# Kernel tuning notes

Measured on AMD Instinct MI355X. Metric: run time of the kernel, lower is better.

## Reference

```python
import jax, jax.numpy as jnp
import numpy as np

V, BLK, L, H, C, FF = 50257, 2048, 6, 8, 512, 2048
D = C // H  # head_dim = 64

def setup_inputs() -> dict:
    key = jax.random.key(0)
    ks = jax.random.split(key, 16)
    s = 0.02
    proj_std = 0.02 / np.sqrt(2 * L)
    return {
        'idx': jax.random.randint(ks[0], (2, 2048), 0, V, dtype=jnp.int64),
        'wte': jax.random.normal(ks[1], (V, C), jnp.float32) * s,
        'wpe': jax.random.normal(ks[2], (BLK, C), jnp.float32) * s,
        'ln1_w': jnp.ones((L, C), jnp.float32), 'ln1_b': jnp.zeros((L, C), jnp.float32),
        'c_attn_w': jax.random.normal(ks[3], (L, 3 * C, C), jnp.float32) * s,
        'c_proj_w': jax.random.normal(ks[4], (L, C, C), jnp.float32) * proj_std,
        'ln2_w': jnp.ones((L, C), jnp.float32), 'ln2_b': jnp.zeros((L, C), jnp.float32),
        'fc_w': jax.random.normal(ks[5], (L, FF, C), jnp.float32) * s,
        'proj_w': jax.random.normal(ks[6], (L, C, FF), jnp.float32) * proj_std,
        'lnf_w': jnp.ones((C,), jnp.float32), 'lnf_b': jnp.zeros((C,), jnp.float32),
    }

def _layernorm(x, w, b, eps=1e-5):
    mu = jnp.mean(x, axis=-1, keepdims=True)
    var = jnp.var(x, axis=-1, keepdims=True)
    return (x - mu) * jax.lax.rsqrt(var + eps) * w + b

def _attn(x, attn_w, proj_w, mask):
    B, T, _ = x.shape
    qkv = jnp.einsum('btc,fc->btf', x, attn_w)  # (B,T,3C)
    q, k, v = jnp.split(qkv, 3, axis=-1)
    q = q.reshape(B, T, H, D)
    k = k.reshape(B, T, H, D)
    v = v.reshape(B, T, H, D)
    scale = 1.0 / np.sqrt(D)
    att = jnp.einsum('bthd,bshd->bhts', q, k) * scale  # (B,H,T,T)
    att = jnp.where(mask, att, -jnp.inf)
    att = jax.nn.softmax(att, axis=-1)
    y = jnp.einsum('bhts,bshd->bthd', att, v).reshape(B, T, C)
    return jnp.einsum('btc,oc->bto', y, proj_w)

def reference(idx, wte, wpe, ln1_w, ln1_b, c_attn_w, c_proj_w, ln2_w, ln2_b, fc_w, proj_w, lnf_w, lnf_b):
    B, T = idx.shape
    pos = jnp.arange(T)
    x = wte[idx] + wpe[pos]  # (B,T,C); dropout p=0
    mask = jnp.tril(jnp.ones((T, T), bool))[None, None]
    for i in range(L):
        x = x + _attn(_layernorm(x, ln1_w[i], ln1_b[i]), c_attn_w[i], c_proj_w[i], mask)
        h = _layernorm(x, ln2_w[i], ln2_b[i])
        h = jax.nn.gelu(jnp.einsum('btc,fc->btf', h, fc_w[i]), approximate=False)
        x = x + jnp.einsum('btf,cf->btc', h, proj_w[i])
    x = _layernorm(x, lnf_w, lnf_b)
    logits = jnp.einsum('btc,vc->btv', x, wte)  # tied lm_head
    return logits
```

## Files before the change

kernel.cpp:

```cpp
#include <hip/hip_runtime.h>

typedef unsigned short u16;
typedef short bf16x8 __attribute__((ext_vector_type(8)));
typedef float f32x4 __attribute__((ext_vector_type(4)));
typedef unsigned short u16x4 __attribute__((ext_vector_type(4)));
typedef unsigned short u16x8 __attribute__((ext_vector_type(8)));
typedef unsigned int u32x2 __attribute__((ext_vector_type(2)));

#define B_ 2
#define T_ 2048
#define C_ 512
#define H_ 8
#define FF_ 2048
#define L_ 6
#define V_ 50257
#define M_ (B_*T_)

__device__ __forceinline__ u16 f2b(float f) {
  union { float f; unsigned u; } v; v.f = f;
  unsigned r = v.u + 0x7FFFu + ((v.u >> 16) & 1u);
  return (u16)(r >> 16);
}
__device__ __forceinline__ float b2f(u16 u) {
  union { unsigned u; float f; } v; v.u = ((unsigned)u) << 16; return v.f;
}
__device__ __forceinline__ unsigned pk_bf16(float lo, float hi) {
  unsigned r;
  asm volatile("v_cvt_pk_bf16_f32 %0, %1, %2" : "=v"(r) : "v"(lo), "v"(hi));
  return r;
}

__device__ __forceinline__ void async16(const void* g, void* l) {
  __builtin_amdgcn_global_load_lds((const __attribute__((address_space(1))) unsigned int*)g,
                                   (__attribute__((address_space(3))) unsigned int*)l, 16, 0, 0);
}

__device__ __forceinline__ bf16x8 scale8(u16x8 v, float s) {
  union { bf16x8 b; unsigned u[4]; } r;
#pragma unroll
  for (int i = 0; i < 4; i++)
    r.u[i] = pk_bf16(b2f(v[2*i]) * s, b2f(v[2*i+1]) * s);
  return r.b;
}

struct CvtArgs { const f32x4* s[5]; u16x4* d[5]; };
__global__ void cvt_all_k(CvtArgs a) {
  const int sizes[5] = { V_*C_/4, L_*3*C_*C_/4, L_*C_*C_/4, L_*FF_*C_/4, L_*C_*FF_/4 };
  int gid = blockIdx.x * blockDim.x + threadIdx.x;
  int stride = gridDim.x * blockDim.x;
#pragma unroll
  for (int seg = 0; seg < 5; seg++) {
    const f32x4* src = a.s[seg];
    u16x4* dst = a.d[seg];
    for (int i = gid; i < sizes[seg]; i += stride) {
      f32x4 v = src[i];
      u16x4 o;
      o[0] = f2b(v[0]); o[1] = f2b(v[1]); o[2] = f2b(v[2]); o[3] = f2b(v[3]);
      dst[i] = o;
    }
  }
}

__global__ void embed_k(const int* __restrict__ idx, const float* __restrict__ wte,
                        const float* __restrict__ wpe, float* __restrict__ x) {
  int t = blockIdx.x * 256 + threadIdx.x;
  int row = t >> 7;
  int c4 = t & 127;
  int tok = idx[row];
  int pos = row & (T_ - 1);
  f32x4 a = ((const f32x4*)(wte + (long)tok * C_))[c4];
  f32x4 p = ((const f32x4*)(wpe + (long)pos * C_))[c4];
  ((f32x4*)x)[t] = a + p;
}

__global__ void ln_k(const float* __restrict__ x, const float* __restrict__ w,
                     const float* __restrict__ b, u16* __restrict__ out) {
  int wv = threadIdx.x >> 6;
  int lane = threadIdx.x & 63;
  int row = blockIdx.x * 4 + wv;
  const f32x4* xr = (const f32x4*)(x + (long)row * C_);
  f32x4 v0 = xr[lane * 2], v1 = xr[lane * 2 + 1];
  float s = 0.f, s2 = 0.f;
#pragma unroll
  for (int j = 0; j < 4; j++) { s += v0[j] + v1[j]; s2 += v0[j]*v0[j] + v1[j]*v1[j]; }
#pragma unroll
  for (int off = 32; off >= 1; off >>= 1) { s += __shfl_xor(s, off); s2 += __shfl_xor(s2, off); }
  float mu = s * (1.f / C_);
  float inv = rsqrtf(s2 * (1.f / C_) - mu * mu + 1e-5f);
  const f32x4* wr = (const f32x4*)w;
  const f32x4* br = (const f32x4*)b;
  f32x4 w0 = wr[lane*2], w1 = wr[lane*2+1], b0 = br[lane*2], b1 = br[lane*2+1];
  u16x8 o;
#pragma unroll
  for (int j = 0; j < 4; j++) {
    o[j]     = f2b((v0[j] - mu) * inv * w0[j] + b0[j]);
    o[j + 4] = f2b((v1[j] - mu) * inv * w1[j] + b1[j]);
  }
  *(u16x8*)(out + (long)row * C_ + lane * 8) = o;
}

template<int EPI, int BM>
__global__ __launch_bounds__(256) void gemm_bt_k(
    const u16* __restrict__ A, const u16* __restrict__ Bw,
    u16* __restrict__ Cb, float* __restrict__ Cf,
    int N, int K, int ldc)
{
  constexpr int MT = BM / 32;
  __shared__ __align__(16) u16 sA[2][BM * 32];
  __shared__ __align__(16) u16 sB[2][128 * 32];
  const int tid = threadIdx.x;
  const int n0 = blockIdx.x * 128;
  const int m0 = blockIdx.y * BM;
  const int w = tid >> 6;
  const int lane = tid & 63;
  const int wm = (w >> 1) * (BM / 2);
  const int wn = (w & 1) * 64;
  const int g = lane >> 4;
  const int l15 = lane & 15;

  f32x4 acc[MT][4] = {};

  const int nk = K >> 5;
  int arow0 = tid >> 2, ak0 = (tid & 3) * 8;
  int c1 = tid + 256;
  int arow1 = c1 >> 2, ak1 = (c1 & 3) * 8;
  const u16* gA0 = A + (long)(m0 + arow0) * K + ak0;
  const u16* gA1 = A + (long)(m0 + arow1) * K + ak1;
  const u16* gB0 = Bw + (long)(n0 + arow0) * K + ak0;
  const u16* gB1 = Bw + (long)(n0 + arow1) * K + ak1;
  const int lb0 = (w * 64) * 8;
  const int lb1 = (256 + w * 64) * 8;

  auto stage = [&](int buf, int kt) {
    int ko = kt << 5;
    async16(gA0 + ko, &sA[buf][lb0]);
    if constexpr (BM == 128) async16(gA1 + ko, &sA[buf][lb1]);
    async16(gB0 + ko, &sB[buf][lb0]);
    async16(gB1 + ko, &sB[buf][lb1]);
  };

  stage(0, 0);
  stage(1, 1);
  for (int kt = 0; kt < nk; kt++) {
    const int cur = kt & 1;
    if (kt + 1 < nk) {
      if constexpr (BM == 128) asm volatile("s_waitcnt vmcnt(4)" ::: "memory");
      else                     asm volatile("s_waitcnt vmcnt(3)" ::: "memory");
    } else {
      asm volatile("s_waitcnt vmcnt(0)" ::: "memory");
    }
    __builtin_amdgcn_s_barrier();
    const u16* pa = sA[cur];
    const u16* pb = sB[cur];
    bf16x8 af[MT], bfr[4];
#pragma unroll
    for (int mt = 0; mt < MT; mt++)
      af[mt] = *(const bf16x8*)(pa + (wm + mt * 16 + l15) * 32 + g * 8);
#pragma unroll
    for (int nt = 0; nt < 4; nt++)
      bfr[nt] = *(const bf16x8*)(pb + (wn + nt * 16 + l15) * 32 + g * 8);
#pragma unroll
    for (int mt = 0; mt < MT; mt++)
#pragma unroll
      for (int nt = 0; nt < 4; nt++)
        acc[mt][nt] = __builtin_amdgcn_mfma_f32_16x16x32_bf16(af[mt], bfr[nt], acc[mt][nt], 0, 0, 0);
    __builtin_amdgcn_s_barrier();
    if (kt + 2 < nk) stage(cur, kt + 2);
  }

#pragma unroll
  for (int mt = 0; mt < MT; mt++) {
    int m = m0 + wm + mt * 16 + g * 4;
#pragma unroll
    for (int nt = 0; nt < 4; nt++) {
      int n = n0 + wn + nt * 16 + l15;
      f32x4 v = acc[mt][nt];
#pragma unroll
      for (int r = 0; r < 4; r++) {
        long ci = (long)(m + r) * ldc + n;
        if (EPI == 0) {
          Cb[ci] = f2b(v[r]);
        } else if (EPI == 1) {
          Cf[ci] += v[r];
        } else {
          float f = v[r];
          f = 0.5f * f * (1.0f + erff(f * 0.70710678118654752f));
          Cb[ci] = f2b(f);
        }
      }
    }
  }
}

__global__ __launch_bounds__(512, 2) void gemm_lmhead_k(
    const u16* __restrict__ A, const u16* __restrict__ Bw,
    float* __restrict__ Cf, int N)
{
  __shared__ __align__(16) u16 sA[2][512 * 32];
  __shared__ __align__(16) u16 sB[2][128 * 32];
  const int K = 512;
  const int bid = blockIdx.x;
  const int swz = (bid & 7) * 393 + (bid >> 3);
  const int n0 = (swz % 393) * 128;
  const int m0 = (swz / 393) * 512;
  const int tid = threadIdx.x;
  const int w = tid >> 6;
  const int lane = tid & 63;
  const int wm = (w >> 1) * 128;
  const int wn = (w & 1) * 64;
  const int g = lane >> 4;
  const int l15 = lane & 15;

  f32x4 acc[8][4] = {};

  const u16* gA[4];
#pragma unroll
  for (int i = 0; i < 4; i++) {
    int c = tid + i * 512;
    gA[i] = A + (long)(m0 + (c >> 2)) * K + (c & 3) * 8;
  }
  int brow = n0 + (tid >> 2); if (brow > N - 1) brow = N - 1;
  const u16* gB0 = Bw + (long)brow * K + (tid & 3) * 8;

  auto stage = [&](int buf, int kt) {
    int ko = kt << 5;
#pragma unroll
    for (int i = 0; i < 4; i++)
      async16(gA[i] + ko, &sA[buf][(i * 512 + w * 64) * 8]);
    async16(gB0 + ko, &sB[buf][(w * 64) * 8]);
  };

  stage(0, 0);
  stage(1, 1);
  const int nk = K >> 5;
  for (int kt = 0; kt < nk; kt++) {
    const int cur = kt & 1;
    if (kt + 1 < nk) asm volatile("s_waitcnt vmcnt(5)" ::: "memory");
    else             asm volatile("s_waitcnt vmcnt(0)" ::: "memory");
    __builtin_amdgcn_s_barrier();
    const u16* pa = sA[cur];
    const u16* pb = sB[cur];
    bf16x8 af[8], bfr[4];
#pragma unroll
    for (int mt = 0; mt < 8; mt++)
      af[mt] = *(const bf16x8*)(pa + (wm + mt * 16 + l15) * 32 + g * 8);
#pragma unroll
    for (int nt = 0; nt < 4; nt++)
      bfr[nt] = *(const bf16x8*)(pb + (wn + nt * 16 + l15) * 32 + g * 8);
    __builtin_amdgcn_s_setprio(1);
#pragma unroll
    for (int mt = 0; mt < 8; mt++)
#pragma unroll
      for (int nt = 0; nt < 4; nt++)
        acc[mt][nt] = __builtin_amdgcn_mfma_f32_16x16x32_bf16(af[mt], bfr[nt], acc[mt][nt], 0, 0, 0);
    __builtin_amdgcn_s_setprio(0);
    __builtin_amdgcn_s_barrier();
    if (kt + 2 < nk) stage(cur, kt + 2);
  }

#pragma unroll
  for (int mt = 0; mt < 8; mt++) {
    int m = m0 + wm + mt * 16 + g * 4;
#pragma unroll
    for (int nt = 0; nt < 4; nt++) {
      int n = n0 + wn + nt * 16 + l15;
      f32x4 v = acc[mt][nt];
      if (n < N) {
#pragma unroll
        for (int r = 0; r < 4; r++)
          Cf[(long)(m + r) * N + n] = v[r];
      }
    }
  }
}

__global__ __launch_bounds__(128) void attn_k(const u16* __restrict__ qkv, u16* __restrict__ out) {
  const int bh = blockIdx.y;
  const int b = bh >> 3;
  const int h = bh & 7;
  const int tid = threadIdx.x;
  const int wv = tid >> 6;
  const int lane = tid & 63;
  const int g = lane >> 4;
  const int l15 = lane & 15;
  const int qblk = 31 - (blockIdx.x >> 1);
  const int halfsel = blockIdx.x & 1;

  __shared__ __align__(16) u16 Ks[2][64 * 64];
  __shared__ __align__(16) u16 Vt[2][64 * 72];
  __shared__ __align__(16) u16 Ps[2][16 * 64];

  const long base = (long)b * T_ * 1536;
  const u16* kbase = qkv + base + 512 + h * 64;
  const u16* vbase = qkv + base + 1024 + h * 64;
  const int kq = tid & 15;
  const int dg = tid >> 4;
  const float qscale = 0.18033688011112042f;

  const int q0 = qblk * 64 + halfsel * 32 + wv * 16;

  const u16* qrow = qkv + base + (long)(q0 + l15) * 1536 + h * 64;
  bf16x8 qf0 = scale8(*(const u16x8*)(qrow + g * 8), qscale);
  bf16x8 qf1 = scale8(*(const u16x8*)(qrow + 32 + g * 8), qscale);

  f32x4 o[4] = {};
  float mrun[4] = {-1e30f, -1e30f, -1e30f, -1e30f};
  float lrun[4] = {0.f, 0.f, 0.f, 0.f};
  const int kvend = qblk * 64 + 64;

  u16x8 vreg[4];
#pragma unroll
  for (int i = 0; i < 4; i++) {
    int chunk = i * 128 + tid;
    int row = chunk >> 3, c8 = chunk & 7;
    async16(kbase + (long)row * 1536 + (c8 ^ (row & 7)) * 8,
            &Ks[0][(i * 128 + wv * 64) * 8]);
  }
#pragma unroll
  for (int t = 0; t < 4; t++)
    vreg[t] = *(const u16x8*)(vbase + (long)(kq + 16 * t) * 1536 + dg * 8);
#pragma unroll
  for (int e = 0; e < 8; e++) {
    int d = dg * 8 + e;
    u32x2 wq = { (unsigned)vreg[0][e] | ((unsigned)vreg[1][e] << 16),
                 (unsigned)vreg[2][e] | ((unsigned)vreg[3][e] << 16) };
    *(u32x2*)(&Vt[0][d * 72 + kq * 4]) = wq;
  }
  __syncthreads();

  int cur = 0;
  for (int j0 = 0; j0 < kvend; j0 += 64, cur ^= 1) {
    const bool more = (j0 + 64) < kvend;
    if (more) {
      int jn = j0 + 64;
#pragma unroll
      for (int i = 0; i < 4; i++) {
        int chunk = i * 128 + tid;
        int row = chunk >> 3, c8 = chunk & 7;
        async16(kbase + (long)(jn + row) * 1536 + (c8 ^ (row & 7)) * 8,
                &Ks[cur ^ 1][(i * 128 + wv * 64) * 8]);
      }
#pragma unroll
      for (int t = 0; t < 4; t++)
        vreg[t] = *(const u16x8*)(vbase + (long)(jn + kq + 16 * t) * 1536 + dg * 8);
    }

    f32x4 s[4] = {};
    const u16* kp = Ks[cur];
#pragma unroll
    for (int t = 0; t < 4; t++) {
      int row = t * 16 + l15;
      const u16* kr = kp + row * 64;
      bf16x8 k0 = *(const bf16x8*)(kr + ((g ^ (row & 7)) * 8));
      bf16x8 k1 = *(const bf16x8*)(kr + (((4 + g) ^ (row & 7)) * 8));
      s[t] = __builtin_amdgcn_mfma_f32_16x16x32_bf16(qf0, k0, s[t], 0, 0, 0);
      s[t] = __builtin_amdgcn_mfma_f32_16x16x32_bf16(qf1, k1, s[t], 0, 0, 0);
    }

    const bool diag = (j0 + 64) == kvend;
    u16* pw = Ps[wv];
#pragma unroll
    for (int r = 0; r < 4; r++) {
      int row = q0 + g * 4 + r;
      float v0 = s[0][r], v1 = s[1][r], v2 = s[2][r], v3 = s[3][r];
      if (diag) {
        if (j0 +      l15 > row) v0 = -1e30f;
        if (j0 + 16 + l15 > row) v1 = -1e30f;
        if (j0 + 32 + l15 > row) v2 = -1e30f;
        if (j0 + 48 + l15 > row) v3 = -1e30f;
      }
      float mloc = fmaxf(fmaxf(v0, v1), fmaxf(v2, v3));
      float m = mrun[r];
      if (!__all(mloc <= m + 8.0f)) {
        float mx = mloc;
        mx = fmaxf(mx, __shfl_xor(mx, 1));
        mx = fmaxf(mx, __shfl_xor(mx, 2));
        mx = fmaxf(mx, __shfl_xor(mx, 4));
        mx = fmaxf(mx, __shfl_xor(mx, 8));
        float mn = fmaxf(m, mx);
        float sc2 = exp2f(m - mn);
        lrun[r] *= sc2;
#pragma unroll
        for (int dt = 0; dt < 4; dt++) o[dt][r] *= sc2;
        m = mn; mrun[r] = mn;
      }
      float e0 = exp2f(v0 - m), e1 = exp2f(v1 - m);
      float e2 = exp2f(v2 - m), e3 = exp2f(v3 - m);
      lrun[r] += (e0 + e1) + (e2 + e3);
      u32x2 pkq = { pk_bf16(e0, e1), pk_bf16(e2, e3) };
      int prow = g * 4 + r;
      int byt = prow * 128 + ((((l15 >> 1) ^ (prow & 7)) << 4)) + (l15 & 1) * 8;
      *(u32x2*)((char*)pw + byt) = pkq;
    }

    const u16* vt = Vt[cur];
    bf16x8 pf0 = *(const bf16x8*)((char*)pw + l15 * 128 + (((g) ^ (l15 & 7)) << 4));
    bf16x8 pf1 = *(const bf16x8*)((char*)pw + l15 * 128 + (((4 + g) ^ (l15 & 7)) << 4));
#pragma unroll
    for (int dt = 0; dt < 4; dt++) {
      int d = dt * 16 + l15;
      bf16x8 vf0 = *(const bf16x8*)(vt + d * 72 + g * 8);
      bf16x8 vf1 = *(const bf16x8*)(vt + d * 72 + 32 + g * 8);
      o[dt] = __builtin_amdgcn_mfma_f32_16x16x32_bf16(pf0, vf0, o[dt], 0, 0, 0);
      o[dt] = __builtin_amdgcn_mfma_f32_16x16x32_bf16(pf1, vf1, o[dt], 0, 0, 0);
    }

    if (more) {
#pragma unroll
      for (int e = 0; e < 8; e++) {
        int d = dg * 8 + e;
        u32x2 wq = { (unsigned)vreg[0][e] | ((unsigned)vreg[1][e] << 16),
                     (unsigned)vreg[2][e] | ((unsigned)vreg[3][e] << 16) };
        *(u32x2*)(&Vt[cur ^ 1][d * 72 + kq * 4]) = wq;
      }
    }
    __syncthreads();
  }

#pragma unroll
  for (int r = 0; r < 4; r++) {
    float ls = lrun[r];
    ls += __shfl_xor(ls, 1); ls += __shfl_xor(ls, 2);
    ls += __shfl_xor(ls, 4); ls += __shfl_xor(ls, 8);
    float inv = 1.0f / ls;
    int row = q0 + g * 4 + r;
    u16* orow = out + (long)(b * T_ + row) * C_ + h * 64;
#pragma unroll
    for (int dt = 0; dt < 4; dt++)
      orow[dt * 16 + l15] = f2b(o[dt][r] * inv);
  }
}

extern "C" void kernel_launch(void* const* d_in, const int* in_sizes, int n_in,
                              void* d_out, int out_size, void* d_ws, size_t ws_size,
                              hipStream_t stream) {
  const int*   idx    = (const int*)  d_in[0];
  const float* wte    = (const float*)d_in[1];
  const float* wpe    = (const float*)d_in[2];
  const float* ln1w   = (const float*)d_in[3];
  const float* ln1b   = (const float*)d_in[4];
  const float* wattn  = (const float*)d_in[5];
  const float* wcproj = (const float*)d_in[6];
  const float* ln2w   = (const float*)d_in[7];
  const float* ln2b   = (const float*)d_in[8];
  const float* wfc    = (const float*)d_in[9];
  const float* wproj2 = (const float*)d_in[10];
  const float* lnfw   = (const float*)d_in[11];
  const float* lnfb   = (const float*)d_in[12];
  float* out = (float*)d_out;

  char* p = (char*)d_ws;
  size_t off = 0;
  auto alloc = [&](size_t bytes) -> void* {
    void* r = p + off; off += (bytes + 255) & ~(size_t)255; return r;
  };
  float* x    = (float*)alloc((size_t)M_ * C_ * 4);
  u16* xn     = (u16*)alloc((size_t)M_ * C_ * 2);
  u16* qkvb   = (u16*)alloc((size_t)M_ * 3 * C_ * 2);
  u16* attb   = (u16*)alloc((size_t)M_ * C_ * 2);
  u16* hb     = (u16*)alloc((size_t)M_ * FF_ * 2);
  u16* wteB   = (u16*)alloc((size_t)V_ * C_ * 2);
  u16* wattnB = (u16*)alloc((size_t)L_ * 3 * C_ * C_ * 2);
  u16* wprojB = (u16*)alloc((size_t)L_ * C_ * C_ * 2);
  u16* wfcB   = (u16*)alloc((size_t)L_ * FF_ * C_ * 2);
  u16* wp2B   = (u16*)alloc((size_t)L_ * C_ * FF_ * 2);
  if (off > ws_size) return;

  CvtArgs ca;
  ca.s[0] = (const f32x4*)wte;    ca.d[0] = (u16x4*)wteB;
  ca.s[1] = (const f32x4*)wattn;  ca.d[1] = (u16x4*)wattnB;
  ca.s[2] = (const f32x4*)wcproj; ca.d[2] = (u16x4*)wprojB;
  ca.s[3] = (const f32x4*)wfc;    ca.d[3] = (u16x4*)wfcB;
  ca.s[4] = (const f32x4*)wproj2; ca.d[4] = (u16x4*)wp2B;
  cvt_all_k<<<dim3(2048), dim3(256), 0, stream>>>(ca);

  embed_k<<<dim3(M_ * C_ / 4 / 256), dim3(256), 0, stream>>>(idx, wte, wpe, x);

  for (int l = 0; l < L_; l++) {
    ln_k<<<dim3(M_ / 4), dim3(256), 0, stream>>>(x, ln1w + l * C_, ln1b + l * C_, xn);
    gemm_bt_k<0, 64><<<dim3(12, 64), dim3(256), 0, stream>>>(
        xn, wattnB + (size_t)l * 3 * C_ * C_, qkvb, nullptr, 3 * C_, C_, 3 * C_);
    attn_k<<<dim3(64, B_ * H_), dim3(128), 0, stream>>>(qkvb, attb);
    gemm_bt_k<1, 64><<<dim3(4, 64), dim3(256), 0, stream>>>(
        attb, wprojB + (size_t)l * C_ * C_, nullptr, x, C_, C_, C_);
    ln_k<<<dim3(M_ / 4), dim3(256), 0, stream>>>(x, ln2w + l * C_, ln2b + l * C_, xn);
    gemm_bt_k<2, 128><<<dim3(16, 32), dim3(256), 0, stream>>>(
        xn, wfcB + (size_t)l * FF_ * C_, hb, nullptr, FF_, C_, FF_);
    gemm_bt_k<1, 64><<<dim3(4, 64), dim3(256), 0, stream>>>(
        hb, wp2B + (size_t)l * C_ * FF_, nullptr, x, C_, FF_, C_);
  }
  ln_k<<<dim3(M_ / 4), dim3(256), 0, stream>>>(x, lnfw, lnfb, xn);
  gemm_lmhead_k<<<dim3(8 * 393), dim3(512), 0, stream>>>(xn, wteB, out, V_);
}
```

Measured before the change: 1.447 ms.

## Triple-buffer GEMM LDS pipelines and shrink tiles for proj and LM-head

Moves both GEMM kernels from double to triple LDS buffering. The next stage is now issued right after the barrier, so the trailing barrier per k-step goes away. Adds a BN template parameter so the residual projection GEMMs use 64x64 tiles, doubling their grid. The LM-head tile is halved to 256x128, which doubles its block count and drops setprio and the occupancy hint. This aims to cut barrier stalls and raise wave occupancy, at the cost of more LDS per block and less reuse per tile in the LM-head.

```diff
diff --git a/kernel.cpp b/kernel.cpp
--- a/kernel.cpp
+++ b/kernel.cpp
@@ -33,6 +33,13 @@
 __device__ __forceinline__ void async16(const void* g, void* l) {
   __builtin_amdgcn_global_load_lds((const __attribute__((address_space(1))) unsigned int*)g,
                                    (__attribute__((address_space(3))) unsigned int*)l, 16, 0, 0);
+}
+
+template<int N> __device__ __forceinline__ void vwait() {
+  if constexpr (N == 0) asm volatile("s_waitcnt vmcnt(0)" ::: "memory");
+  else if constexpr (N == 2) asm volatile("s_waitcnt vmcnt(2)" ::: "memory");
+  else if constexpr (N == 3) asm volatile("s_waitcnt vmcnt(3)" ::: "memory");
+  else if constexpr (N == 4) asm volatile("s_waitcnt vmcnt(4)" ::: "memory");
 }
 
 __device__ __forceinline__ bf16x8 scale8(u16x8 v, float s) {
@@ -99,80 +106,82 @@
   *(u16x8*)(out + (long)row * C_ + lane * 8) = o;
 }
 
-template<int EPI, int BM>
+template<int EPI, int BM, int BN>
 __global__ __launch_bounds__(256) void gemm_bt_k(
     const u16* __restrict__ A, const u16* __restrict__ Bw,
     u16* __restrict__ Cb, float* __restrict__ Cf,
     int N, int K, int ldc)
 {
   constexpr int MT = BM / 32;
-  __shared__ __align__(16) u16 sA[2][BM * 32];
-  __shared__ __align__(16) u16 sB[2][128 * 32];
+  constexpr int NT = BN / 32;
+  constexpr int AJ = BM / 64;
+  constexpr int BJ = BN / 64;
+  constexpr int LPT = AJ + BJ;
+  __shared__ __align__(16) u16 sA[3][BM * 32];
+  __shared__ __align__(16) u16 sB[3][BN * 32];
   const int tid = threadIdx.x;
-  const int n0 = blockIdx.x * 128;
+  const int n0 = blockIdx.x * BN;
   const int m0 = blockIdx.y * BM;
   const int w = tid >> 6;
   const int lane = tid & 63;
   const int wm = (w >> 1) * (BM / 2);
-  const int wn = (w & 1) * 64;
+  const int wn = (w & 1) * (BN / 2);
   const int g = lane >> 4;
   const int l15 = lane & 15;
 
-  f32x4 acc[MT][4] = {};
+  f32x4 acc[MT][NT] = {};
 
   const int nk = K >> 5;
-  int arow0 = tid >> 2, ak0 = (tid & 3) * 8;
-  int c1 = tid + 256;
-  int arow1 = c1 >> 2, ak1 = (c1 & 3) * 8;
-  const u16* gA0 = A + (long)(m0 + arow0) * K + ak0;
-  const u16* gA1 = A + (long)(m0 + arow1) * K + ak1;
-  const u16* gB0 = Bw + (long)(n0 + arow0) * K + ak0;
-  const u16* gB1 = Bw + (long)(n0 + arow1) * K + ak1;
-  const int lb0 = (w * 64) * 8;
-  const int lb1 = (256 + w * 64) * 8;
+  const int k8 = (tid & 3) * 8;
+  const u16* gA[AJ];
+  const u16* gB[BJ];
+#pragma unroll
+  for (int j = 0; j < AJ; j++)
+    gA[j] = A + (long)(m0 + (tid >> 2) + j * 64) * K + k8;
+#pragma unroll
+  for (int j = 0; j < BJ; j++)
+    gB[j] = Bw + (long)(n0 + (tid >> 2) + j * 64) * K + k8;
 
   auto stage = [&](int buf, int kt) {
     int ko = kt << 5;
-    async16(gA0 + ko, &sA[buf][lb0]);
-    if constexpr (BM == 128) async16(gA1 + ko, &sA[buf][lb1]);
-    async16(gB0 + ko, &sB[buf][lb0]);
-    async16(gB1 + ko, &sB[buf][lb1]);
+#pragma unroll
+    for (int j = 0; j < AJ; j++)
+      async16(gA[j] + ko, &sA[buf][(j * 256 + w * 64) * 8]);
+#pragma unroll
+    for (int j = 0; j < BJ; j++)
+      async16(gB[j] + ko, &sB[buf][(j * 256 + w * 64) * 8]);
   };
 
   stage(0, 0);
   stage(1, 1);
+  int cur = 0, nxt = 2;
   for (int kt = 0; kt < nk; kt++) {
-    const int cur = kt & 1;
-    if (kt + 1 < nk) {
-      if constexpr (BM == 128) asm volatile("s_waitcnt vmcnt(4)" ::: "memory");
-      else                     asm volatile("s_waitcnt vmcnt(3)" ::: "memory");
-    } else {
-      asm volatile("s_waitcnt vmcnt(0)" ::: "memory");
-    }
+    if (kt + 1 < nk) vwait<LPT>(); else vwait<0>();
     __builtin_amdgcn_s_barrier();
+    if (kt + 2 < nk) stage(nxt, kt + 2);
     const u16* pa = sA[cur];
     const u16* pb = sB[cur];
-    bf16x8 af[MT], bfr[4];
+    bf16x8 af[MT], bfr[NT];
 #pragma unroll
     for (int mt = 0; mt < MT; mt++)
       af[mt] = *(const bf16x8*)(pa + (wm + mt * 16 + l15) * 32 + g * 8);
 #pragma unroll
-    for (int nt = 0; nt < 4; nt++)
+    for (int nt = 0; nt < NT; nt++)
       bfr[nt] = *(const bf16x8*)(pb + (wn + nt * 16 + l15) * 32 + g * 8);
 #pragma unroll
     for (int mt = 0; mt < MT; mt++)
 #pragma unroll
-      for (int nt = 0; nt < 4; nt++)
+      for (int nt = 0; nt < NT; nt++)
         acc[mt][nt] = __builtin_amdgcn_mfma_f32_16x16x32_bf16(af[mt], bfr[nt], acc[mt][nt], 0, 0, 0);
-    __builtin_amdgcn_s_barrier();
-    if (kt + 2 < nk) stage(cur, kt + 2);
+    cur = (cur == 2) ? 0 : cur + 1;
+    nxt = (nxt == 2) ? 0 : nxt + 1;
   }
 
 #pragma unroll
   for (int mt = 0; mt < MT; mt++) {
     int m = m0 + wm + mt * 16 + g * 4;
 #pragma unroll
-    for (int nt = 0; nt < 4; nt++) {
+    for (int nt = 0; nt < NT; nt++) {
       int n = n0 + wn + nt * 16 + l15;
       f32x4 v = acc[mt][nt];
 #pragma unroll
@@ -192,74 +201,71 @@
   }
 }
 
-__global__ __launch_bounds__(512, 2) void gemm_lmhead_k(
+__global__ __launch_bounds__(512) void gemm_lmhead_k(
     const u16* __restrict__ A, const u16* __restrict__ Bw,
     float* __restrict__ Cf, int N)
 {
-  __shared__ __align__(16) u16 sA[2][512 * 32];
-  __shared__ __align__(16) u16 sB[2][128 * 32];
+  __shared__ __align__(16) u16 sA[3][256 * 32];
+  __shared__ __align__(16) u16 sB[3][128 * 32];
   const int K = 512;
   const int bid = blockIdx.x;
-  const int swz = (bid & 7) * 393 + (bid >> 3);
+  const int swz = (bid & 7) * 786 + (bid >> 3);
   const int n0 = (swz % 393) * 128;
-  const int m0 = (swz / 393) * 512;
+  const int m0 = (swz / 393) * 256;
   const int tid = threadIdx.x;
   const int w = tid >> 6;
   const int lane = tid & 63;
-  const int wm = (w >> 1) * 128;
+  const int wm = (w >> 1) * 64;
   const int wn = (w & 1) * 64;
   const int g = lane >> 4;
   const int l15 = lane & 15;
 
-  f32x4 acc[8][4] = {};
-
-  const u16* gA[4];
-#pragma unroll
-  for (int i = 0; i < 4; i++) {
-    int c = tid + i * 512;
-    gA[i] = A + (long)(m0 + (c >> 2)) * K + (c & 3) * 8;
-  }
+  f32x4 acc[4][4] = {};
+
+  const int k8 = (tid & 3) * 8;
+  const u16* gA[2];
+#pragma unroll
+  for (int j = 0; j < 2; j++)
+    gA[j] = A + (long)(m0 + (tid >> 2) + j * 128) * K + k8;
   int brow = n0 + (tid >> 2); if (brow > N - 1) brow = N - 1;
-  const u16* gB0 = Bw + (long)brow * K + (tid & 3) * 8;
+  const u16* gB0 = Bw + (long)brow * K + k8;
 
   auto stage = [&](int buf, int kt) {
     int ko = kt << 5;
 #pragma unroll
-    for (int i = 0; i < 4; i++)
-      async16(gA[i] + ko, &sA[buf][(i * 512 + w * 64) * 8]);
+    for (int j = 0; j < 2; j++)
+      async16(gA[j] + ko, &sA[buf][(j * 512 + w * 64) * 8]);
     async16(gB0 + ko, &sB[buf][(w * 64) * 8]);
   };
 
   stage(0, 0);
   stage(1, 1);
+  int cur = 0, nxt = 2;
   const int nk = K >> 5;
   for (int kt = 0; kt < nk; kt++) {
-    const int cur = kt & 1;
-    if (kt + 1 < nk) asm volatile("s_waitcnt vmcnt(5)" ::: "memory");
-    else             asm volatile("s_waitcnt vmcnt(0)" ::: "memory");
+    if (kt + 1 < nk) vwait<3>(); else vwait<0>();
     __builtin_amdgcn_s_barrier();
+    if (kt + 2 < nk) stage(nxt, kt + 2);
     const u16* pa = sA[cur];
     const u16* pb = sB[cur];
-    bf16x8 af[8], bfr[4];
-#pragma unroll
-    for (int mt = 0; mt < 8; mt++)
+    bf16x8 af[4], bfr[4];
+#pragma unroll
+    for (int mt = 0; mt < 4; mt++)
       af[mt] = *(const bf16x8*)(pa + (wm + mt * 16 + l15) * 32 + g * 8);
 #pragma unroll
     for (int nt = 0; nt < 4; nt++)
       bfr[nt] = *(const bf16x8*)(pb + (wn + nt * 16 + l15) * 32 + g * 8);
-    __builtin_amdgcn_s_setprio(1);
-#pragma unroll
-    for (int mt = 0; mt < 8; mt++)
+#pragma unroll
+    for (int mt = 0; mt < 4; mt++)
 #pragma unroll
       for (int nt = 0; nt < 4; nt++)
         acc[mt][nt] = __builtin_amdgcn_mfma_f32_16x16x32_bf16(af[mt], bfr[nt], acc[mt][nt], 0, 0, 0);
-    __builtin_amdgcn_s_setprio(0);
-    __builtin_amdgcn_s_barrier();
-    if (kt + 2 < nk) stage(cur, kt + 2);
-  }
-
-#pragma unroll
-  for (int mt = 0; mt < 8; mt++) {
+    cur = (cur == 2) ? 0 : cur + 1;
+    nxt = (nxt == 2) ? 0 : nxt + 1;
+  }
+
+#pragma unroll
+  for (int mt = 0; mt < 4; mt++) {
     int m = m0 + wm + mt * 16 + g * 4;
 #pragma unroll
     for (int nt = 0; nt < 4; nt++) {
@@ -478,17 +484,17 @@
 
   for (int l = 0; l < L_; l++) {
     ln_k<<<dim3(M_ / 4), dim3(256), 0, stream>>>(x, ln1w + l * C_, ln1b + l * C_, xn);
-    gemm_bt_k<0, 64><<<dim3(12, 64), dim3(256), 0, stream>>>(
+    gemm_bt_k<0, 64, 128><<<dim3(12, 64), dim3(256), 0, stream>>>(
         xn, wattnB + (size_t)l * 3 * C_ * C_, qkvb, nullptr, 3 * C_, C_, 3 * C_);
     attn_k<<<dim3(64, B_ * H_), dim3(128), 0, stream>>>(qkvb, attb);
-    gemm_bt_k<1, 64><<<dim3(4, 64), dim3(256), 0, stream>>>(
+    gemm_bt_k<1, 64, 64><<<dim3(8, 64), dim3(256), 0, stream>>>(
         attb, wprojB + (size_t)l * C_ * C_, nullptr, x, C_, C_, C_);
     ln_k<<<dim3(M_ / 4), dim3(256), 0, stream>>>(x, ln2w + l * C_, ln2b + l * C_, xn);
-    gemm_bt_k<2, 128><<<dim3(16, 32), dim3(256), 0, stream>>>(
+    gemm_bt_k<2, 128, 128><<<dim3(16, 32), dim3(256), 0, stream>>>(
         xn, wfcB + (size_t)l * FF_ * C_, hb, nullptr, FF_, C_, FF_);
-    gemm_bt_k<1, 64><<<dim3(4, 64), dim3(256), 0, stream>>>(
+    gemm_bt_k<1, 64, 64><<<dim3(8, 64), dim3(256), 0, stream>>>(
         hb, wp2B + (size_t)l * C_ * FF_, nullptr, x, C_, FF_, C_);
   }
   ln_k<<<dim3(M_ / 4), dim3(256), 0, stream>>>(x, lnfw, lnfb, xn);
-  gemm_lmhead_k<<<dim3(8 * 393), dim3(512), 0, stream>>>(xn, wteB, out, V_);
-}
+  gemm_lmhead_k<<<dim3(8 * 786), dim3(512), 0, stream>>>(xn, wteB, out, V_);
+}
```

Measured after the change: 1.374 ms. -5.0%, faster.
